# Kernel optimization log

Measured on AMD Instinct MI355X. Metric: run time of the kernel, lower is better.

Reference implementation:

```python
import jax, jax.numpy as jnp
import numpy as np
from jax import lax


def _conv2d_same(x, w, b):
    # NHWC input, HWIO kernel, stride 1, SAME padding (matches keras Conv2D)
    y = lax.conv_general_dilated(x, w, window_strides=(1, 1), padding='SAME',
                                 dimension_numbers=('NHWC', 'HWIO', 'NHWC'))
    return y + b


def setup_inputs() -> dict:
    key = jax.random.key(0)
    k1, k2, k3, k4 = jax.random.split(key, 4)
    B, H, W, C = 16, 128, 128, 256
    F = 256
    inputs = jax.random.normal(k1, (B, H, W, C), dtype=jnp.float32)
    # offset conv: small random weights so offsets are non-trivial but in-range-ish
    w_off = jax.random.normal(k2, (3, 3, C, 2), dtype=jnp.float32) * 0.05
    b_off = jnp.zeros((2,), dtype=jnp.float32)
    w_def = jax.random.normal(k3, (3, 3, C, F), dtype=jnp.float32) * (1.0 / np.sqrt(9 * C))
    b_def = jax.random.normal(k4, (F,), dtype=jnp.float32) * 0.01
    return {"inputs": inputs, "w_off": w_off, "b_off": b_off,
            "w_def": w_def, "b_def": b_def}


def reference(inputs, w_off, b_off, w_def, b_def):
    B, H, W, C = inputs.shape
    # 1) predict per-pixel (dy, dx) offsets
    offsets = _conv2d_same(inputs, w_off, b_off)          # (B,H,W,2)
    off_h = offsets[..., 0]                               # (B,H,W)
    off_w = offsets[..., 1]                               # (B,H,W)
    # 2) build sampling grid, add offsets, clip, truncate to int (tf.cast semantics;
    #    values are non-negative after clip so truncation == floor)
    yy, xx = jnp.meshgrid(jnp.arange(H, dtype=inputs.dtype),
                          jnp.arange(W, dtype=inputs.dtype), indexing='ij')
    y = jnp.clip(yy[None] + off_h, 0.0, H - 1).astype(jnp.int32)   # (B,H,W)
    x = jnp.clip(xx[None] + off_w, 0.0, W - 1).astype(jnp.int32)   # (B,H,W)
    # 3) gather: one offset per pixel, shared across all channels
    lin = (y * W + x).reshape(B, H * W, 1)                # (B,HW,1)
    sampled = jnp.take_along_axis(inputs.reshape(B, H * W, C), lin, axis=1)
    sampled = sampled.reshape(B, H, W, C)
    # 4) main conv on resampled features
    return _conv2d_same(sampled, w_def, b_def)
```

## Files before the change

### kernel.cpp

```cpp
#include <hip/hip_runtime.h>
#include <hip/hip_bf16.h>

typedef __attribute__((ext_vector_type(8))) short bf16x8;
typedef __attribute__((ext_vector_type(4))) float f32x4;

__device__ __forceinline__ unsigned short f2bf(float f) {
  __hip_bfloat16 h = __float2bfloat16(f);
  return *reinterpret_cast<unsigned short*>(&h);
}

__device__ __forceinline__ void gld_lds16(void* lds, const void* g) {
  __builtin_amdgcn_global_load_lds(
      (const __attribute__((address_space(1))) unsigned int*)g,
      (__attribute__((address_space(3))) unsigned int*)lds, 16, 0, 0);
}

__global__ __launch_bounds__(256) void k1_offs_gather(
    const float* __restrict__ in, const float* __restrict__ w_off,
    const float* __restrict__ b_off, unsigned short* __restrict__ samp) {
  __shared__ float tile[3][128][34];
  __shared__ float wlf[9 * 64];
  __shared__ double dsum[2][128][2];
  __shared__ int lin_lds[128];

  const int bid = blockIdx.x;
  const int b = bid >> 7, h = bid & 127;
  const int t = threadIdx.x;
  const int w = t & 127, half = t >> 7, ch0 = half * 16;

  double a0 = 0.0, a1 = 0.0;

  for (int c0 = 0; c0 < 256; c0 += 32) {
    __syncthreads();
    for (int i = t; i < 576; i += 256) {
      int tap = i >> 6, r = i & 63;
      wlf[i] = w_off[tap * 512 + c0 * 2 + r];
    }
    for (int dr = 0; dr < 3; ++dr) {
      int hh = h + dr - 1;
      if ((unsigned)hh < 128u) {
        const float* rbase = in + ((size_t)(b * 128 + hh) * 128) * 256 + c0;
        #pragma unroll
        for (int it = 0; it < 4; ++it) {
          int idx = it * 256 + t;
          int ww = idx >> 3, cq = idx & 7;
          const float4 v = *(const float4*)(rbase + ww * 256 + cq * 4);
          float* dst = &tile[dr][ww][cq * 4];
          *(float2*)dst = make_float2(v.x, v.y);
          *(float2*)(dst + 2) = make_float2(v.z, v.w);
        }
      } else {
        #pragma unroll
        for (int it = 0; it < 4; ++it) {
          int idx = it * 256 + t;
          int ww = idx >> 3, cq = idx & 7;
          float* dst = &tile[dr][ww][cq * 4];
          *(float2*)dst = make_float2(0.f, 0.f);
          *(float2*)(dst + 2) = make_float2(0.f, 0.f);
        }
      }
    }
    __syncthreads();
    #pragma unroll
    for (int dr = 0; dr < 3; ++dr) {
      #pragma unroll
      for (int dc = 0; dc < 3; ++dc) {
        int wsrc = w + dc - 1;
        if ((unsigned)wsrc >= 128u) continue;
        const float2* tp2 = (const float2*)&tile[dr][wsrc][ch0];
        const float2* wp2 = (const float2*)&wlf[(dr * 3 + dc) * 64 + ch0 * 2];
        #pragma unroll
        for (int c2 = 0; c2 < 8; ++c2) {
          float2 v = tp2[c2];
          float2 wa = wp2[2 * c2];
          float2 wb = wp2[2 * c2 + 1];
          a0 += (double)v.x * (double)wa.x;
          a1 += (double)v.x * (double)wa.y;
          a0 += (double)v.y * (double)wb.x;
          a1 += (double)v.y * (double)wb.y;
        }
      }
    }
  }
  dsum[half][w][0] = a0;
  dsum[half][w][1] = a1;
  __syncthreads();
  if (t < 128) {
    double o0 = dsum[0][t][0] + dsum[1][t][0] + (double)b_off[0];
    double o1 = dsum[0][t][1] + dsum[1][t][1] + (double)b_off[1];
    double yd = (double)h + o0;
    double xd = (double)t + o1;
    yd = yd < 0.0 ? 0.0 : (yd > 127.0 ? 127.0 : yd);
    xd = xd < 0.0 ? 0.0 : (xd > 127.0 ? 127.0 : xd);
    int y = (int)yd, x = (int)xd;
    lin_lds[t] = y * 128 + x;
  }
  __syncthreads();
  const float* imgbase = in + (size_t)b * 16384 * 256;
  unsigned short* obase = samp + (size_t)bid * 128 * 256;
  for (int it = 0; it < 32; ++it) {
    int idx = it * 256 + t;
    int px = idx >> 6, cv = idx & 63;
    const float4 v = *(const float4*)(imgbase + (size_t)lin_lds[px] * 256 + cv * 4);
    ushort4 o;
    o.x = f2bf(v.x); o.y = f2bf(v.y); o.z = f2bf(v.z); o.w = f2bf(v.w);
    *(ushort4*)(obase + px * 256 + cv * 4) = o;
  }
}

__global__ __launch_bounds__(256) void k2_wT(const float* __restrict__ wdef,
                                             unsigned short* __restrict__ wT) {
  int g = blockIdx.x * 256 + threadIdx.x;
  int tap = g >> 16;
  int n = (g >> 8) & 255;
  int k = g & 255;
  wT[g] = f2bf(wdef[((size_t)tap * 256 + k) * 256 + n]);
}

__global__ __launch_bounds__(512, 2) void k3_conv(
    const unsigned short* __restrict__ samp, const unsigned short* __restrict__ wT,
    const float* __restrict__ b_def, float* __restrict__ out,
    const unsigned short* __restrict__ zerobuf) {
  __shared__ __align__(16) unsigned char smem[131072];

  const int bid0 = blockIdx.x;
  const int mt = (bid0 & 7) * 128 + (bid0 >> 3);
  const int bimg = mt >> 6;
  const int h0 = (mt & 63) * 2;

  const int tid = threadIdx.x;
  const int lane = tid & 63, wave = tid >> 6;
  const int wr = wave >> 2, wc = wave & 3;
  const int r15 = lane & 15, g4 = lane >> 4;
  const int g4eff = g4 ^ ((r15 >> 1) & 3);

  int aoff[8], boff[4];
  #pragma unroll
  for (int mi = 0; mi < 8; ++mi)
    aoff[mi] = (wr * 128 + mi * 16 + r15) * 32 + g4eff * 8;
  #pragma unroll
  for (int ni = 0; ni < 4; ++ni)
    boff[ni] = (wc * 64 + ni * 16 + r15) * 32 + g4eff * 8;

  f32x4 acc[8][4];
  #pragma unroll
  for (int i = 0; i < 8; ++i)
    #pragma unroll
    for (int j = 0; j < 4; ++j) acc[i][j] = (f32x4){0.f, 0.f, 0.f, 0.f};

  auto stage = [&](int ts) {
    const int tap = ts >> 3, kc2 = ts & 7;
    const int q = (tap * 11) >> 5;
    const int dr = q - 1, dc = tap - q * 3 - 1;
    unsigned char* Ad = smem + (size_t)(ts & 3) * 16384;
    unsigned char* Bd = smem + 65536 + (size_t)(ts & 3) * 16384;
    const unsigned short* bt = wT + tap * 65536 + kc2 * 32;
    #pragma unroll
    for (int it = 0; it < 2; ++it) {
      const int slot = it * 512 + tid;
      const int i = slot >> 2, ch = slot & 3;
      const int chs = ch ^ ((i >> 1) & 3);
      const int hh = h0 + (i >> 7) + dr;
      const int ww = (i & 127) + dc;
      const unsigned short* src =
          ((unsigned)hh < 128u && (unsigned)ww < 128u)
              ? (samp + ((size_t)(bimg * 128 + hh) * 128 + ww) * 256 + kc2 * 32 + chs * 8)
              : (zerobuf + ch * 8);
      gld_lds16(Ad + slot * 16, src);
    }
    #pragma unroll
    for (int it = 0; it < 2; ++it) {
      const int slot = it * 512 + tid;
      const int n = slot >> 2, ch = slot & 3;
      const int chs = ch ^ ((n >> 1) & 3);
      gld_lds16(Bd + slot * 16, bt + n * 256 + chs * 8);
    }
  };

  auto compute = [&](int T) {
    const unsigned short* Ab = (const unsigned short*)(smem + (size_t)(T & 3) * 16384);
    const unsigned short* Bb = (const unsigned short*)(smem + 65536 + (size_t)(T & 3) * 16384);
    bf16x8 af[8], bfr[4];
    #pragma unroll
    for (int mi = 0; mi < 8; ++mi) af[mi] = *(const bf16x8*)(Ab + aoff[mi]);
    #pragma unroll
    for (int ni = 0; ni < 4; ++ni) bfr[ni] = *(const bf16x8*)(Bb + boff[ni]);
    __builtin_amdgcn_s_setprio(1);
    #pragma unroll
    for (int mi = 0; mi < 8; ++mi)
      #pragma unroll
      for (int ni = 0; ni < 4; ++ni)
        acc[mi][ni] = __builtin_amdgcn_mfma_f32_16x16x32_bf16(
            af[mi], bfr[ni], acc[mi][ni], 0, 0, 0);
    __builtin_amdgcn_s_setprio(0);
  };

#define K3_STEP(T, VM)                                      \
  {                                                         \
    if ((T) + 3 < 72) stage((T) + 3);                       \
    asm volatile("s_waitcnt vmcnt(" #VM ")" ::: "memory");  \
    __builtin_amdgcn_s_barrier();                           \
    __builtin_amdgcn_sched_barrier(0);                      \
    compute(T);                                             \
    asm volatile("" ::: "memory");                          \
    __builtin_amdgcn_sched_barrier(0);                      \
    __builtin_amdgcn_s_barrier();                           \
  }

  stage(0); stage(1); stage(2);
  for (int t = 0; t < 69; ++t) K3_STEP(t, 12);
  K3_STEP(69, 8);
  K3_STEP(70, 4);
  K3_STEP(71, 0);
#undef K3_STEP

  const int colg = wc * 64 + r15;
  float bias[4];
  #pragma unroll
  for (int ni = 0; ni < 4; ++ni) bias[ni] = b_def[colg + ni * 16];
  #pragma unroll
  for (int mi = 0; mi < 8; ++mi) {
    const int r0 = wr * 128 + mi * 16 + g4 * 4;
    #pragma unroll
    for (int j = 0; j < 4; ++j) {
      float* orow = out + ((size_t)mt * 256 + r0 + j) * 256 + colg;
      #pragma unroll
      for (int ni = 0; ni < 4; ++ni) orow[ni * 16] = acc[mi][ni][j] + bias[ni];
    }
  }
}

extern "C" void kernel_launch(void* const* d_in, const int* in_sizes, int n_in,
                              void* d_out, int out_size, void* d_ws, size_t ws_size,
                              hipStream_t stream) {
  const float* in = (const float*)d_in[0];
  const float* w_off = (const float*)d_in[1];
  const float* b_off = (const float*)d_in[2];
  const float* w_def = (const float*)d_in[3];
  const float* b_def = (const float*)d_in[4];
  float* out = (float*)d_out;

  char* ws = (char*)d_ws;
  unsigned short* zerobuf = (unsigned short*)ws;
  unsigned short* wT = (unsigned short*)(ws + 4096);
  unsigned short* samp = (unsigned short*)(ws + 4096 + 1179648);

  hipMemsetAsync(ws, 0, 4096, stream);
  hipLaunchKernelGGL(k2_wT, dim3(2304), dim3(256), 0, stream, w_def, wT);
  hipLaunchKernelGGL(k1_offs_gather, dim3(2048), dim3(256), 0, stream,
                     in, w_off, b_off, samp);
  hipLaunchKernelGGL(k3_conv, dim3(1024), dim3(512), 0, stream,
                     samp, wT, b_def, out, zerobuf);
}
```

Baseline: 539.7 us.

## Restructure conv GEMM main loop to one barrier per K-step

The main GEMM loop is split into a fragment read from LDS and an MFMA phase. Each step now reads its fragments first, then issues the async global-to-LDS loads for step t+3 into the free ring slot, then runs the MFMAs. It ends with a single vmcnt wait and one barrier instead of two barriers per step. This is meant to cut synchronisation stalls and overlap the load issue with the matrix math, at the cost of holding fragment registers across the load-issue phase and relying on the four-slot ring for safety.

```diff
diff --git a/kernel.cpp b/kernel.cpp
--- a/kernel.cpp
+++ b/kernel.cpp
@@ -177,14 +177,16 @@
     }
   };
 
-  auto compute = [&](int T) {
+  auto readfrags = [&](int T, bf16x8* af, bf16x8* bfr) {
     const unsigned short* Ab = (const unsigned short*)(smem + (size_t)(T & 3) * 16384);
     const unsigned short* Bb = (const unsigned short*)(smem + 65536 + (size_t)(T & 3) * 16384);
-    bf16x8 af[8], bfr[4];
     #pragma unroll
     for (int mi = 0; mi < 8; ++mi) af[mi] = *(const bf16x8*)(Ab + aoff[mi]);
     #pragma unroll
     for (int ni = 0; ni < 4; ++ni) bfr[ni] = *(const bf16x8*)(Bb + boff[ni]);
+  };
+
+  auto mfma32 = [&](bf16x8* af, bf16x8* bfr) {
     __builtin_amdgcn_s_setprio(1);
     #pragma unroll
     for (int mi = 0; mi < 8; ++mi)
@@ -195,24 +197,49 @@
     __builtin_amdgcn_s_setprio(0);
   };
 
-#define K3_STEP(T, VM)                                      \
-  {                                                         \
-    if ((T) + 3 < 72) stage((T) + 3);                       \
-    asm volatile("s_waitcnt vmcnt(" #VM ")" ::: "memory");  \
-    __builtin_amdgcn_s_barrier();                           \
-    __builtin_amdgcn_sched_barrier(0);                      \
-    compute(T);                                             \
-    asm volatile("" ::: "memory");                          \
-    __builtin_amdgcn_sched_barrier(0);                      \
-    __builtin_amdgcn_s_barrier();                           \
-  }
-
   stage(0); stage(1); stage(2);
-  for (int t = 0; t < 69; ++t) K3_STEP(t, 12);
-  K3_STEP(69, 8);
-  K3_STEP(70, 4);
-  K3_STEP(71, 0);
-#undef K3_STEP
+  asm volatile("s_waitcnt vmcnt(8)" ::: "memory");
+  __builtin_amdgcn_s_barrier();
+  asm volatile("" ::: "memory");
+  __builtin_amdgcn_sched_barrier(0);
+
+  for (int t = 0; t < 69; ++t) {
+    bf16x8 af[8], bfr[4];
+    readfrags(t, af, bfr);
+    stage(t + 3);
+    __builtin_amdgcn_sched_barrier(0);
+    mfma32(af, bfr);
+    asm volatile("s_waitcnt vmcnt(8)" ::: "memory");
+    __builtin_amdgcn_s_barrier();
+    asm volatile("" ::: "memory");
+    __builtin_amdgcn_sched_barrier(0);
+  }
+  {
+    bf16x8 af[8], bfr[4];
+    readfrags(69, af, bfr);
+    __builtin_amdgcn_sched_barrier(0);
+    mfma32(af, bfr);
+    asm volatile("s_waitcnt vmcnt(4)" ::: "memory");
+    __builtin_amdgcn_s_barrier();
+    asm volatile("" ::: "memory");
+    __builtin_amdgcn_sched_barrier(0);
+  }
+  {
+    bf16x8 af[8], bfr[4];
+    readfrags(70, af, bfr);
+    __builtin_amdgcn_sched_barrier(0);
+    mfma32(af, bfr);
+    asm volatile("s_waitcnt vmcnt(0)" ::: "memory");
+    __builtin_amdgcn_s_barrier();
+    asm volatile("" ::: "memory");
+    __builtin_amdgcn_sched_barrier(0);
+  }
+  {
+    bf16x8 af[8], bfr[4];
+    readfrags(71, af, bfr);
+    __builtin_amdgcn_sched_barrier(0);
+    mfma32(af, bfr);
+  }
 
   const int colg = wc * 64 + r15;
   float bias[4];
```

Measured after the change: 525.0 us. 1.03x faster.
